# Optimization experiments

Measured on AMD Instinct MI355X. Metric: run time of the kernel, lower is better.

Reference implementation:

```python
import jax, jax.numpy as jnp
import numpy as np

# Spiking-neuron constants (ALIF_Neuron / output_Neuron are not in the given
# source; we use the standard surrogate-gradient spiking update from this repo
# family: mem = prev*decay*(1-spike) + input; spike = Heaviside(mem-thresh)).
THRESH = 0.5
LENS = 0.5
DECAY = 0.2

B, T, I, H = 64, 512, 256, 512

@jax.custom_vjp
def spike_fn(v):
    return (v > THRESH).astype(v.dtype)

def _spike_fwd(v):
    return spike_fn(v), v

def _spike_bwd(v, g):
    sg = (jnp.abs(v - THRESH) < LENS).astype(v.dtype) / (2.0 * LENS)
    return (g * sg,)

spike_fn.defvjp(_spike_fwd, _spike_bwd)


def setup_inputs() -> dict:
    key = jax.random.key(0)
    ks = jax.random.split(key, 7)
    sc = 0.05
    return {
        "x": jax.random.normal(ks[0], (B, T, I), jnp.float32),
        "Wx0": jax.random.normal(ks[1], (I, 4 * H), jnp.float32) * sc,
        "Wh0": jax.random.normal(ks[2], (H, 4 * H), jnp.float32) * sc,
        "bh0": jax.random.normal(ks[3], (4 * H,), jnp.float32) * sc,
        "Wx1": jax.random.normal(ks[4], (H, 4 * H), jnp.float32) * sc,
        "Wh1": jax.random.normal(ks[5], (H, 4 * H), jnp.float32) * sc,
        "bh1": jax.random.normal(ks[6], (4 * H,), jnp.float32) * sc,
    }


def _cell(xt, s, h, c, Wx, Wh, bh, is_output):
    # ifgo: [B, 4H]; chunk order i, f, g, o as in the torch code
    ifgo = xt @ Wx + h @ Wh + bh
    i, f, g, o = jnp.split(ifgo, 4, axis=-1)
    c_next = jax.nn.sigmoid(f) * c + jax.nn.sigmoid(i) * jnp.tanh(g)
    h_next = jax.nn.sigmoid(o) * jnp.tanh(c_next)
    if is_output:
        # output_Neuron(x, h_next): leaky integration of membrane with input
        h_next = h_next * DECAY + xt
        return s, h_next, c_next
    # ALIF_Neuron(s, h_next, s): adaptive mem update + surrogate spike
    mem = s * DECAY * (1.0 - s) + h_next
    s_new = spike_fn(mem)
    return s_new, mem, c_next


def reference(x, Wx0, Wh0, bh0, Wx1, Wh1, bh1):
    Bb = x.shape[0]
    z = jnp.zeros((Bb, H), x.dtype)
    init = (z, z, z, z, z, z)  # s0, h0, c0, s1, h1, c1

    def step(carry, xt):
        s0, h0, c0, s1, h1, c1 = carry
        s0, h0, c0 = _cell(xt, s0, h0, c0, Wx0, Wh0, bh0, False)
        # layer 1 consumes the spike output s0 of layer 0
        s1, h1, c1 = _cell(s0, s1, h1, c1, Wx1, Wh1, bh1, True)
        return (s0, h0, c0, s1, h1, c1), h1

    xs = jnp.swapaxes(x, 0, 1)  # [T, B, I]
    carry, outs = jax.lax.scan(step, init, xs)
    out = jnp.swapaxes(outs, 0, 1)  # [B, T, H] (batch_first)
    s0, h0, c0, s1, h1, c1 = carry
    s = jnp.stack([s0, s1])
    h = jnp.stack([h0, h1])
    c = jnp.stack([c0, c1])
    return out, s, h, c
```

## Files before the change

kernel.cpp:

```cpp
#include <hip/hip_runtime.h>
#include <math.h>

typedef float vf4 __attribute__((ext_vector_type(4)));

constexpr int T  = 512;
constexpr int BB = 64;
constexpr int II = 256;
constexpr int HH = 512;

constexpr int SOFF = BB * T * HH;
constexpr int HOFF = SOFF + 2 * BB * HH;
constexpr int COFF = HOFF + 2 * BB * HH;

constexpr int WS_WC0 = 0;
constexpr int WS_WC1 = 1572864;
constexpr int WS_BH0 = 3670016;
constexpr int WS_BH1 = 3672064;
constexpr int WS_HX0 = 3674112;
constexpr int WS_HX1 = 3739648;
constexpr int WS_SX  = 3805184;
constexpr int WS_FLG = 3809280;

__device__ __forceinline__ void bypass_st(float* p, float v) {
  asm volatile("global_store_dword %0, %1, off sc0 sc1" :: "v"(p), "v"(v) : "memory");
}
__device__ __forceinline__ void bypass_st_u32(unsigned* p, unsigned v) {
  asm volatile("global_store_dword %0, %1, off sc0 sc1" :: "v"(p), "v"(v) : "memory");
}
__device__ __forceinline__ void bypass_st_u8(unsigned char* p, unsigned v) {
  asm volatile("global_store_byte %0, %1, off sc0 sc1" :: "v"(p), "v"(v) : "memory");
}
__device__ __forceinline__ unsigned bypass_ldu(const unsigned* p) {
  unsigned r;
  asm volatile("global_load_dword %0, %1, off sc0 sc1\n\ts_waitcnt vmcnt(0)"
               : "=v"(r) : "v"(p) : "memory");
  return r;
}
__device__ __forceinline__ unsigned long long bypass_ld64(const unsigned long long* p) {
  unsigned long long r;
  asm volatile("global_load_dwordx2 %0, %1, off sc0 sc1\n\ts_waitcnt vmcnt(0)"
               : "=v"(r) : "v"(p) : "memory");
  return r;
}
__device__ __forceinline__ void bypass_ld2x4(const vf4* p0, const vf4* p1, vf4& r0, vf4& r1) {
  asm volatile(
      "global_load_dwordx4 %0, %2, off sc0 sc1\n\t"
      "global_load_dwordx4 %1, %3, off sc0 sc1\n\t"
      "s_waitcnt vmcnt(0)"
      : "=&v"(r0), "=&v"(r1) : "v"(p0), "v"(p1) : "memory");
}

__device__ __forceinline__ float sigf(float x) { return 1.0f / (1.0f + __expf(-x)); }
__device__ __forceinline__ float tanh_fast(float x) {
  return 1.0f - 2.0f / (1.0f + __expf(2.0f * x));
}

__device__ __forceinline__ float sxor(float v, int m) { return __shfl_xor(v, m, 64); }
__device__ __forceinline__ vf4 sxor4(vf4 v, int m) {
  vf4 r; r.x = sxor(v.x, m); r.y = sxor(v.y, m); r.z = sxor(v.z, m); r.w = sxor(v.w, m);
  return r;
}

__device__ __forceinline__ int rev3(int v) {
  return ((v & 1) << 2) | (v & 2) | ((v >> 2) & 1);
}

__device__ __forceinline__ vf4 reduce8(const vf4* acc, int kl) {
  const int sel = kl & 1;
  vf4 n0[4];
#pragma unroll
  for (int i = 0; i < 4; ++i) {
    vf4 snd = sel ? acc[i] : acc[i + 4];
    vf4 kp  = sel ? acc[i + 4] : acc[i];
    n0[i] = kp + sxor4(snd, 1);
  }
  const int sel2 = (kl >> 1) & 1;
  vf4 n1[2];
#pragma unroll
  for (int i = 0; i < 2; ++i) {
    vf4 snd = sel2 ? n0[i] : n0[i + 2];
    vf4 kp  = sel2 ? n0[i + 2] : n0[i];
    n1[i] = kp + sxor4(snd, 2);
  }
  const int sel3 = (kl >> 2) & 1;
  vf4 snd = sel3 ? n1[0] : n1[1];
  vf4 kp  = sel3 ? n1[1] : n1[0];
  vf4 r = kp + sxor4(snd, 4);
  r += sxor4(r, 8);
  r += sxor4(r, 16);
  r += sxor4(r, 32);
  return r;
}

__global__ void pack_wc(const float* __restrict__ A, const float* __restrict__ B,
                        int Ka, int K, float* __restrict__ Wp) {
  const int j = blockIdx.x;
  for (int k = threadIdx.x; k < K; k += 256) {
    const float* src = (k < Ka) ? (A + (size_t)k * 2048) : (B + (size_t)(k - Ka) * 2048);
    vf4 v = {src[j], src[512 + j], src[1024 + j], src[1536 + j]};
    ((vf4*)Wp)[(size_t)j * K + k] = v;
  }
}

__global__ void pack_bias(const float* __restrict__ bh0, const float* __restrict__ bh1,
                          float* __restrict__ bh0p, float* __restrict__ bh1p) {
  const int i = blockIdx.x * blockDim.x + threadIdx.x;
  if (i < 2048) {
    bh0p[i] = bh0[(i & 3) * 512 + (i >> 2)];
  } else {
    int q = i - 2048;
    bh1p[q] = bh1[(q & 3) * 512 + (q >> 2)];
  }
}

__global__ __launch_bounds__(1024, 1) void aslstm_main(
    const vf4* __restrict__ Wc0p, const vf4* __restrict__ Wc1p,
    const vf4* __restrict__ bh0p, const vf4* __restrict__ bh1p,
    const float* __restrict__ x,
    float* __restrict__ hx0, float* __restrict__ hx1,
    unsigned char* __restrict__ sxb,
    unsigned* __restrict__ flags,
    float* __restrict__ out) {
  const int wg  = blockIdx.x;
  const int xcd = wg & 7;
  const int a   = wg >> 3;
  const int g   = a & 7;
  const int s   = (a >> 3) * 8 + xcd;
  const int tid = threadIdx.x;
  const int jo  = tid >> 6;
  const int kl  = tid & 63;
  const int j   = s * 16 + jo;
  const int b_loc  = rev3(kl & 7);
  const int b_glob = g * 8 + b_loc;
  const bool rep0  = (kl < 8);

  __shared__ float cat0[8][776];
  __shared__ float cat1[8][1032];
  __shared__ unsigned long long swords[64];

  float c0 = 0.0f, c1 = 0.0f, sp = 0.0f;

  const int sb2 = tid >> 7;
  const int sj2 = (tid & 127) * 4;

  {
    if (tid < 512) {
      int bx = tid >> 6, kx = (tid & 63) * 4;
      *(vf4*)&cat0[bx][kx] = *(const vf4*)&x[(size_t)(g * 8 + bx) * (T * II) + kx];
    }
    const vf4* hp = (const vf4*)(hx0 + 32768 + g * 4096 + sb2 * 512 + sj2);
    vf4 r0, r1;  bypass_ld2x4(hp, hp, r0, r1);
    *(vf4*)&cat0[sb2][256 + sj2] = r0;
  }
  __syncthreads();

  for (int t = 0; t < T; ++t) {
    vf4 acc[8];
#pragma unroll
    for (int b = 0; b < 8; ++b) acc[b] = vf4{0, 0, 0, 0};
    {
      const vf4* wr = Wc0p + (size_t)j * 768;
#pragma unroll
      for (int ig = 0; ig < 3; ++ig) {
        const int k0 = ig * 256 + kl * 4;
        vf4 w0 = wr[k0], w1 = wr[k0 + 1], w2 = wr[k0 + 2], w3 = wr[k0 + 3];
#pragma unroll
        for (int b = 0; b < 8; ++b) {
          vf4 av = *(const vf4*)&cat0[b][k0];
          acc[b] += av.x * w0; acc[b] += av.y * w1;
          acc[b] += av.z * w2; acc[b] += av.w * w3;
        }
      }
    }

    {
      vf4 p = reduce8(acc, kl) + bh0p[j];
      float cn  = sigf(p.y) * c0 + sigf(p.x) * tanh_fast(p.z);
      float mem = sigf(p.w) * tanh_fast(cn);
      float sn  = (mem > 0.5f) ? 1.0f : 0.0f;
      c0 = cn; sp = sn;
      unsigned long long ball = __ballot(sn != 0.0f);
      if (rep0) {
        bypass_st(&hx0[(t & 1) * 32768 + g * 4096 + b_loc * 512 + j], mem);
        if (kl == 0)
          bypass_st_u8(&sxb[(size_t)(t & 3) * 4096 + g * 512 + j],
                       (unsigned)(ball & 0xFFull));
        if (t == T - 1) {
          out[SOFF + b_glob * 512 + j] = sn;
          out[HOFF + b_glob * 512 + j] = mem;
          out[COFF + b_glob * 512 + j] = cn;
        }
      }
    }
    __syncthreads();

    if (tid == 0) bypass_st_u32(&flags[g * 64 + s], (unsigned)(t + 1));
    if (tid < 64) {
      const unsigned tgt = (unsigned)(t + 1);
      for (;;) {
        unsigned v = bypass_ldu(&flags[g * 64 + (tid & 31)]);
        if (__all((int)(v >= tgt))) break;
        __builtin_amdgcn_s_sleep(1);
      }
      swords[tid] = bypass_ld64(
          (const unsigned long long*)(sxb + (size_t)(t & 3) * 4096 + g * 512) + tid);
    }
    __syncthreads();

    {
      const vf4* hp1 = (const vf4*)(hx1 + ((t + 1) & 1) * 32768 + g * 4096 + sb2 * 512 + sj2);
      const vf4* hp0 = (const vf4*)(hx0 + (t & 1) * 32768 + g * 4096 + sb2 * 512 + sj2);
      vf4 r1, r0;  bypass_ld2x4(hp1, hp0, r1, r0);
      *(vf4*)&cat1[sb2][512 + sj2] = r1;
      *(vf4*)&cat0[sb2][256 + sj2] = r0;

      if (tid < 512) {
        const int jd = tid;
        unsigned byte = ((const unsigned char*)swords)[jd];
#pragma unroll
        for (int b = 0; b < 8; ++b)
          cat1[b][jd] = (float)((byte >> rev3(b)) & 1u);

        if (t < T - 1) {
          int bx = tid >> 6, kx = (tid & 63) * 4;
          *(vf4*)&cat0[bx][kx] =
              *(const vf4*)&x[(size_t)(g * 8 + bx) * (T * II) + (size_t)(t + 1) * II + kx];
        }
      }
    }
    __syncthreads();

#pragma unroll
    for (int b = 0; b < 8; ++b) acc[b] = vf4{0, 0, 0, 0};
    {
      const vf4* wr = Wc1p + (size_t)j * 1024;
#pragma unroll
      for (int ig = 0; ig < 4; ++ig) {
        const int k0 = ig * 256 + kl * 4;
        vf4 w0 = wr[k0], w1 = wr[k0 + 1], w2 = wr[k0 + 2], w3 = wr[k0 + 3];
#pragma unroll
        for (int b = 0; b < 8; ++b) {
          vf4 av = *(const vf4*)&cat1[b][k0];
          acc[b] += av.x * w0; acc[b] += av.y * w1;
          acc[b] += av.z * w2; acc[b] += av.w * w3;
        }
      }
    }

    {
      vf4 p = reduce8(acc, kl) + bh1p[j];
      float cn  = sigf(p.y) * c1 + sigf(p.x) * tanh_fast(p.z);
      float hn  = sigf(p.w) * tanh_fast(cn);
      float h1n = hn * 0.2f + sp;
      c1 = cn;
      if (rep0) {
        bypass_st(&hx1[(t & 1) * 32768 + g * 4096 + b_loc * 512 + j], h1n);
        out[(size_t)b_glob * (T * HH) + (size_t)t * HH + j] = h1n;
        if (t == T - 1) {
          out[HOFF + 32768 + b_glob * 512 + j] = h1n;
          out[COFF + 32768 + b_glob * 512 + j] = cn;
        }
      }
    }
  }
}

extern "C" void kernel_launch(void* const* d_in, const int* in_sizes, int n_in,
                              void* d_out, int out_size, void* d_ws, size_t ws_size,
                              hipStream_t stream) {
  const float* x   = (const float*)d_in[0];
  const float* Wx0 = (const float*)d_in[1];
  const float* Wh0 = (const float*)d_in[2];
  const float* bh0 = (const float*)d_in[3];
  const float* Wx1 = (const float*)d_in[4];
  const float* Wh1 = (const float*)d_in[5];
  const float* bh1 = (const float*)d_in[6];
  float* out = (float*)d_out;
  float* ws  = (float*)d_ws;

  float* Wc0p  = ws + WS_WC0;
  float* Wc1p  = ws + WS_WC1;
  float* bh0pf = ws + WS_BH0;
  float* bh1pf = ws + WS_BH1;
  float* hx0   = ws + WS_HX0;
  float* hx1   = ws + WS_HX1;
  unsigned char* sxb = (unsigned char*)(ws + WS_SX);
  unsigned* flags = (unsigned*)(ws + WS_FLG);

  hipMemsetAsync(hx0, 0, 2 * 64 * 512 * sizeof(float), stream);
  hipMemsetAsync(hx1, 0, 2 * 64 * 512 * sizeof(float), stream);
  hipMemsetAsync(sxb, 0, 16384, stream);
  hipMemsetAsync(flags, 0, 512 * sizeof(unsigned), stream);
  hipMemsetAsync(out + SOFF + BB * HH, 0, BB * HH * sizeof(float), stream);

  pack_wc<<<dim3(512), dim3(256), 0, stream>>>(Wx0, Wh0, 256, 768, Wc0p);
  pack_wc<<<dim3(512), dim3(256), 0, stream>>>(Wx1, Wh1, 512, 1024, Wc1p);
  pack_bias<<<dim3(16), dim3(256), 0, stream>>>(bh0, bh1, bh0pf, bh1pf);

  aslstm_main<<<dim3(256), dim3(1024), 0, stream>>>(
      (const vf4*)Wc0p, (const vf4*)Wc1p, (const vf4*)bh0pf, (const vf4*)bh1pf,
      x, hx0, hx1, sxb, flags, out);
}
```

Baseline: 8.947 ms.

## Rework per-step exchange: drop spike bitmask, per-warp polling, transposed hidden layout

Removes the separate spike-byte buffer and its ballot/store. Spikes are now recomputed from the exchanged membrane values by thresholding, and the hidden-state exchange buffers are stored batch-minor, so each lane loads a contiguous slice for its own block of columns. Every warp now polls one producer flag itself instead of one warp polling all flags and then a second barrier. This removes one barrier per step, and the next-step x load is issued before the barrier to overlap its latency. The trade-off is more redundant flag polling traffic and scattered LDS scalar writes.

Measured after the change: 8.139 ms. 1.1x faster.

```diff
diff --git a/kernel.cpp b/kernel.cpp
--- a/kernel.cpp
+++ b/kernel.cpp
@@ -18,7 +18,6 @@
 constexpr int WS_BH1 = 3672064;
 constexpr int WS_HX0 = 3674112;
 constexpr int WS_HX1 = 3739648;
-constexpr int WS_SX  = 3805184;
 constexpr int WS_FLG = 3809280;
 
 __device__ __forceinline__ void bypass_st(float* p, float v) {
@@ -26,20 +25,11 @@
 }
 __device__ __forceinline__ void bypass_st_u32(unsigned* p, unsigned v) {
   asm volatile("global_store_dword %0, %1, off sc0 sc1" :: "v"(p), "v"(v) : "memory");
-}
-__device__ __forceinline__ void bypass_st_u8(unsigned char* p, unsigned v) {
-  asm volatile("global_store_byte %0, %1, off sc0 sc1" :: "v"(p), "v"(v) : "memory");
 }
 __device__ __forceinline__ unsigned bypass_ldu(const unsigned* p) {
   unsigned r;
   asm volatile("global_load_dword %0, %1, off sc0 sc1\n\ts_waitcnt vmcnt(0)"
-               : "=v"(r) : "v"(p) : "memory");
-  return r;
-}
-__device__ __forceinline__ unsigned long long bypass_ld64(const unsigned long long* p) {
-  unsigned long long r;
-  asm volatile("global_load_dwordx2 %0, %1, off sc0 sc1\n\ts_waitcnt vmcnt(0)"
-               : "=v"(r) : "v"(p) : "memory");
+               : "=&v"(r) : "v"(p) : "memory");
   return r;
 }
 __device__ __forceinline__ void bypass_ld2x4(const vf4* p0, const vf4* p1, vf4& r0, vf4& r1) {
@@ -48,6 +38,9 @@
       "global_load_dwordx4 %1, %3, off sc0 sc1\n\t"
       "s_waitcnt vmcnt(0)"
       : "=&v"(r0), "=&v"(r1) : "v"(p0), "v"(p1) : "memory");
+}
+__device__ __forceinline__ void release_drain() {
+  asm volatile("s_waitcnt vmcnt(0)" ::: "memory");
 }
 
 __device__ __forceinline__ float sigf(float x) { return 1.0f / (1.0f + __expf(-x)); }
@@ -118,7 +111,6 @@
     const vf4* __restrict__ bh0p, const vf4* __restrict__ bh1p,
     const float* __restrict__ x,
     float* __restrict__ hx0, float* __restrict__ hx1,
-    unsigned char* __restrict__ sxb,
     unsigned* __restrict__ flags,
     float* __restrict__ out) {
   const int wg  = blockIdx.x;
@@ -136,21 +128,23 @@
 
   __shared__ float cat0[8][776];
   __shared__ float cat1[8][1032];
-  __shared__ unsigned long long swords[64];
 
   float c0 = 0.0f, c1 = 0.0f, sp = 0.0f;
 
-  const int sb2 = tid >> 7;
-  const int sj2 = (tid & 127) * 4;
-
+  const int pl = (jo << 1) | (kl >> 5);
+  const int lc = kl & 31;
+  const int js = pl * 16 + (lc >> 1);
+  const int b0 = (lc & 1) * 4;
+  const int fo = g * 4096 + pl * 128 + lc * 4;
+  const bool poller = ((kl & 31) == 0);
+
+  if (tid < 512) {
+    int bx = tid >> 6, kx = (tid & 63) * 4;
+    *(vf4*)&cat0[bx][kx] = *(const vf4*)&x[(size_t)(g * 8 + bx) * (T * II) + kx];
+  }
   {
-    if (tid < 512) {
-      int bx = tid >> 6, kx = (tid & 63) * 4;
-      *(vf4*)&cat0[bx][kx] = *(const vf4*)&x[(size_t)(g * 8 + bx) * (T * II) + kx];
-    }
-    const vf4* hp = (const vf4*)(hx0 + 32768 + g * 4096 + sb2 * 512 + sj2);
-    vf4 r0, r1;  bypass_ld2x4(hp, hp, r0, r1);
-    *(vf4*)&cat0[sb2][256 + sj2] = r0;
+    int bz = tid >> 7, kz = (tid & 127) * 4;
+    *(vf4*)&cat0[bz][256 + kz] = vf4{0.0f, 0.0f, 0.0f, 0.0f};
   }
   __syncthreads();
 
@@ -179,12 +173,8 @@
       float mem = sigf(p.w) * tanh_fast(cn);
       float sn  = (mem > 0.5f) ? 1.0f : 0.0f;
       c0 = cn; sp = sn;
-      unsigned long long ball = __ballot(sn != 0.0f);
       if (rep0) {
-        bypass_st(&hx0[(t & 1) * 32768 + g * 4096 + b_loc * 512 + j], mem);
-        if (kl == 0)
-          bypass_st_u8(&sxb[(size_t)(t & 3) * 4096 + g * 512 + j],
-                       (unsigned)(ball & 0xFFull));
+        bypass_st(&hx0[(t & 1) * 32768 + g * 4096 + j * 8 + b_loc], mem);
         if (t == T - 1) {
           out[SOFF + b_glob * 512 + j] = sn;
           out[HOFF + b_glob * 512 + j] = mem;
@@ -192,40 +182,45 @@
         }
       }
     }
+
+    vf4 xv = vf4{0, 0, 0, 0};
+    if (tid < 512 && t < T - 1) {
+      int bx = tid >> 6, kx = (tid & 63) * 4;
+      xv = *(const vf4*)&x[(size_t)(g * 8 + bx) * (T * II) + (size_t)(t + 1) * II + kx];
+    }
+
+    release_drain();
     __syncthreads();
-
     if (tid == 0) bypass_st_u32(&flags[g * 64 + s], (unsigned)(t + 1));
-    if (tid < 64) {
+
+    {
       const unsigned tgt = (unsigned)(t + 1);
+      const unsigned* fp = &flags[g * 64 + pl];
       for (;;) {
-        unsigned v = bypass_ldu(&flags[g * 64 + (tid & 31)]);
+        unsigned v = tgt;
+        if (poller) v = bypass_ldu(fp);
         if (__all((int)(v >= tgt))) break;
         __builtin_amdgcn_s_sleep(1);
       }
-      swords[tid] = bypass_ld64(
-          (const unsigned long long*)(sxb + (size_t)(t & 3) * 4096 + g * 512) + tid);
-    }
-    __syncthreads();
-
-    {
-      const vf4* hp1 = (const vf4*)(hx1 + ((t + 1) & 1) * 32768 + g * 4096 + sb2 * 512 + sj2);
-      const vf4* hp0 = (const vf4*)(hx0 + (t & 1) * 32768 + g * 4096 + sb2 * 512 + sj2);
-      vf4 r1, r0;  bypass_ld2x4(hp1, hp0, r1, r0);
-      *(vf4*)&cat1[sb2][512 + sj2] = r1;
-      *(vf4*)&cat0[sb2][256 + sj2] = r0;
-
+      const vf4* mp = (const vf4*)(hx0 + (t & 1) * 32768 + fo);
+      const vf4* hp = (const vf4*)(hx1 + ((t + 1) & 1) * 32768 + fo);
+      vf4 mv, hv;
+      bypass_ld2x4(mp, hp, mv, hv);
+      cat0[b0 + 0][256 + js] = mv.x;
+      cat0[b0 + 1][256 + js] = mv.y;
+      cat0[b0 + 2][256 + js] = mv.z;
+      cat0[b0 + 3][256 + js] = mv.w;
+      cat1[b0 + 0][js] = (mv.x > 0.5f) ? 1.0f : 0.0f;
+      cat1[b0 + 1][js] = (mv.y > 0.5f) ? 1.0f : 0.0f;
+      cat1[b0 + 2][js] = (mv.z > 0.5f) ? 1.0f : 0.0f;
+      cat1[b0 + 3][js] = (mv.w > 0.5f) ? 1.0f : 0.0f;
+      cat1[b0 + 0][512 + js] = hv.x;
+      cat1[b0 + 1][512 + js] = hv.y;
+      cat1[b0 + 2][512 + js] = hv.z;
+      cat1[b0 + 3][512 + js] = hv.w;
       if (tid < 512) {
-        const int jd = tid;
-        unsigned byte = ((const unsigned char*)swords)[jd];
-#pragma unroll
-        for (int b = 0; b < 8; ++b)
-          cat1[b][jd] = (float)((byte >> rev3(b)) & 1u);
-
-        if (t < T - 1) {
-          int bx = tid >> 6, kx = (tid & 63) * 4;
-          *(vf4*)&cat0[bx][kx] =
-              *(const vf4*)&x[(size_t)(g * 8 + bx) * (T * II) + (size_t)(t + 1) * II + kx];
-        }
+        int bx = tid >> 6, kx = (tid & 63) * 4;
+        *(vf4*)&cat0[bx][kx] = xv;
       }
     }
     __syncthreads();
@@ -254,7 +249,7 @@
       float h1n = hn * 0.2f + sp;
       c1 = cn;
       if (rep0) {
-        bypass_st(&hx1[(t & 1) * 32768 + g * 4096 + b_loc * 512 + j], h1n);
+        bypass_st(&hx1[(t & 1) * 32768 + g * 4096 + j * 8 + b_loc], h1n);
         out[(size_t)b_glob * (T * HH) + (size_t)t * HH + j] = h1n;
         if (t == T - 1) {
           out[HOFF + 32768 + b_glob * 512 + j] = h1n;
@@ -284,12 +279,10 @@
   float* bh1pf = ws + WS_BH1;
   float* hx0   = ws + WS_HX0;
   float* hx1   = ws + WS_HX1;
-  unsigned char* sxb = (unsigned char*)(ws + WS_SX);
   unsigned* flags = (unsigned*)(ws + WS_FLG);
 
   hipMemsetAsync(hx0, 0, 2 * 64 * 512 * sizeof(float), stream);
   hipMemsetAsync(hx1, 0, 2 * 64 * 512 * sizeof(float), stream);
-  hipMemsetAsync(sxb, 0, 16384, stream);
   hipMemsetAsync(flags, 0, 512 * sizeof(unsigned), stream);
   hipMemsetAsync(out + SOFF + BB * HH, 0, BB * HH * sizeof(float), stream);
 
@@ -299,5 +292,5 @@
 
   aslstm_main<<<dim3(256), dim3(1024), 0, stream>>>(
       (const vf4*)Wc0p, (const vf4*)Wc1p, (const vf4*)bh0pf, (const vf4*)bh1pf,
-      x, hx0, hx1, sxb, flags, out);
-}
+      x, hx0, hx1, flags, out);
+}
```
